# Optimization experiments

Hardware: AMD Instinct MI355X
Metric: run time of the kernel (lower is better)

Reference implementation:

```python
import jax, jax.numpy as jnp
import numpy as np

B, IN_DIM, H1, H2, C = 8192, 1024, 2048, 2048, 1000
E, TOP_K, RH = 8, 2, 512
QB = 127.0
EPS = 1e-5


def _ste_round(x):
    # straight-through estimator round (BitNet-style)
    return x + jax.lax.stop_gradient(jnp.round(x) - x)


def _act_quant(x):
    # per-token absmax 8-bit activation quantization
    s = QB / jnp.clip(jnp.max(jnp.abs(x), axis=-1, keepdims=True), EPS, None)
    return jnp.clip(_ste_round(x * s), -QB, QB) / s


def _weight_quant(w):
    # ternary 1.58b weight quantization, per-tensor mean-abs scale
    s = jnp.clip(jnp.mean(jnp.abs(w)), EPS, None)
    return jnp.clip(_ste_round(w / s), -1.0, 1.0) * s


def _bit_linear(x, w, b):
    return _act_quant(x) @ _weight_quant(w).T + b


def setup_inputs() -> dict:
    key = jax.random.key(0)
    ks = jax.random.split(key, 12)
    def init(k, shape, fan_in):
        return (jax.random.normal(k, shape, dtype=jnp.float32) / np.sqrt(fan_in)).astype(jnp.float32)
    return {
        "x":  jax.random.normal(ks[0], (B, IN_DIM), dtype=jnp.float32),
        "Wr1": init(ks[1], (RH, IN_DIM), IN_DIM),
        "br1": jnp.zeros((RH,), jnp.float32),
        "Wr2": init(ks[2], (E, RH), RH),
        "br2": jnp.zeros((E,), jnp.float32),
        "W1": init(ks[3], (E, H1, IN_DIM), IN_DIM),
        "b1": jnp.zeros((E, H1), jnp.float32),
        "W2": init(ks[4], (E, H2, H1), H1),
        "b2": jnp.zeros((E, H2), jnp.float32),
        "W3": init(ks[5], (E, C, H2), H2),
        "b3": jnp.zeros((E, C), jnp.float32),
    }


def _forward(x, Wr1, br1, Wr2, br2, W1, b1, W2, b2, W3, b3):
    # Router (eval mode: dropout off)
    h = jax.nn.relu(x @ Wr1.T + br1)
    router_probs = jax.nn.softmax(h @ Wr2.T + br2, axis=1)       # [B, E]
    topk_vals, topk_idx = jax.lax.top_k(router_probs, TOP_K)     # [B, K]

    # dense gate matrix: gate[b,e] = sum_k topk_vals[b,k] * (topk_idx[b,k]==e)
    gates = jnp.sum(topk_vals[..., None] * jax.nn.one_hot(topk_idx, E, dtype=x.dtype), axis=1)  # [B, E]

    def expert(w1, c1, w2, c2, w3, c3):
        y = jax.nn.relu(_bit_linear(x, w1, c1))
        y = jax.nn.relu(_bit_linear(y, w2, c2))
        return _bit_linear(y, w3, c3)                             # [B, C]

    out_all = jax.vmap(expert)(W1, b1, W2, b2, W3, b3)            # [E, B, C]
    outputs = jnp.einsum('ebc,be->bc', out_all, gates) / TOP_K    # [B, C]
    load_balancing_loss = jnp.zeros((), x.dtype)                  # eval mode
    return outputs, router_probs, load_balancing_loss


def reference(x, Wr1, br1, Wr2, br2, W1, b1, W2, b2, W3, b3):
    return _forward(x, Wr1, br1, Wr2, br2, W1, b1, W2, b2, W3, b3)
```

## Files before the change

### kernel.cpp

```cpp
#include <hip/hip_runtime.h>
#include <stdint.h>

#define DEV static __device__ __forceinline__

typedef int v4i __attribute__((ext_vector_type(4)));
typedef short v8s __attribute__((ext_vector_type(8)));
typedef float v4f __attribute__((ext_vector_type(4)));

constexpr int B_T   = 8192;
constexpr int IN_D  = 1024;
constexpr int H1D   = 2048;
constexpr int H2D   = 2048;
constexpr int CDIM  = 1000;
constexpr int NEXP  = 8;
constexpr int RHD   = 512;
constexpr float QBF  = 127.0f;
constexpr float EPSF = 1e-5f;
constexpr int NSLOT = 2 * B_T;
constexpr int MAXT  = 136;
constexpr float GAP_DELTA = 2e-3f;

DEV void load_lds16(const void* g, void* l) {
  __builtin_amdgcn_global_load_lds(
      (const __attribute__((address_space(1))) uint32_t*)(uintptr_t)g,
      (__attribute__((address_space(3))) uint32_t*)(uint32_t)(uintptr_t)l,
      16, 0, 0);
}

DEV uint32_t pack4(float a, float b, float c, float d, float s) {
  int q0 = (int)rintf(a * s); q0 = q0 > 127 ? 127 : (q0 < -127 ? -127 : q0);
  int q1 = (int)rintf(b * s); q1 = q1 > 127 ? 127 : (q1 < -127 ? -127 : q1);
  int q2 = (int)rintf(c * s); q2 = q2 > 127 ? 127 : (q2 < -127 ? -127 : q2);
  int q3 = (int)rintf(d * s); q3 = q3 > 127 ? 127 : (q3 < -127 ? -127 : q3);
  return (uint32_t)(uint8_t)q0 | ((uint32_t)(uint8_t)q1 << 8) |
         ((uint32_t)(uint8_t)q2 << 16) | ((uint32_t)(uint8_t)q3 << 24);
}

DEV uint16_t f2bf(float f) {
  uint32_t u = __float_as_uint(f);
  return (uint16_t)((u + 0x7FFFu + ((u >> 16) & 1u)) >> 16);
}
DEV float bf2f(uint16_t h) { return __uint_as_float((uint32_t)h << 16); }

__global__ __launch_bounds__(256) void wabs_reduce(const float* __restrict__ W,
                                                   long perExpert, int tbase,
                                                   double* __restrict__ partial) {
  int e = blockIdx.y;
  const float4* base = (const float4*)(W + (long)e * perExpert);
  long n4 = perExpert >> 2;
  double s = 0.0;
  for (long i = (long)blockIdx.x * 256 + threadIdx.x; i < n4; i += 32L * 256L) {
    float4 v = base[i];
    s += (double)fabsf(v.x) + (double)fabsf(v.y) + (double)fabsf(v.z) + (double)fabsf(v.w);
  }
  __shared__ double red[256];
  red[threadIdx.x] = s;
  __syncthreads();
  for (int st = 128; st > 0; st >>= 1) {
    if ((int)threadIdx.x < st) red[threadIdx.x] += red[threadIdx.x + st];
    __syncthreads();
  }
  if (threadIdx.x == 0) partial[(long)(tbase + e) * 32 + blockIdx.x] = red[0];
}

__global__ void finalize_scales(const double* __restrict__ partial, float* __restrict__ swf) {
  int t = threadIdx.x;
  if (t >= 24) return;
  double s = 0.0;
  for (int i = 0; i < 32; ++i) s += partial[t * 32 + i];
  long cnt = (t < 8) ? (long)H1D * IN_D : (t < 16) ? (long)H2D * H1D : (long)CDIM * H2D;
  float mean = (float)(s / (double)cnt);
  swf[t] = fmaxf(mean, EPSF);
}

__global__ __launch_bounds__(256) void wquant(const float* __restrict__ W,
                                              int8_t* __restrict__ Wq,
                                              const float* __restrict__ swf, int tbase,
                                              long perExpert, long total4) {
  long i = (long)blockIdx.x * 256 + threadIdx.x;
  if (i >= total4) return;
  long e = (i * 4) / perExpert;
  float s = swf[tbase + (int)e];
  float4 v = ((const float4*)W)[i];
  float t0 = fminf(fmaxf(rintf(v.x / s), -1.f), 1.f);
  float t1 = fminf(fmaxf(rintf(v.y / s), -1.f), 1.f);
  float t2 = fminf(fmaxf(rintf(v.z / s), -1.f), 1.f);
  float t3 = fminf(fmaxf(rintf(v.w / s), -1.f), 1.f);
  uint32_t p = (uint32_t)(uint8_t)(int8_t)t0 | ((uint32_t)(uint8_t)(int8_t)t1 << 8) |
               ((uint32_t)(uint8_t)(int8_t)t2 << 16) | ((uint32_t)(uint8_t)(int8_t)t3 << 24);
  ((uint32_t*)Wq)[i] = p;
}

template <int WIDTH>
__global__ __launch_bounds__(256) void actquant(const float* __restrict__ X,
                                                int8_t* __restrict__ Xq,
                                                float* __restrict__ rcp_out) {
  constexpr int PT = WIDTH / 1024;
  const int row = blockIdx.x;
  const int tid = threadIdx.x;
  const float4* src = (const float4*)(X + (size_t)row * WIDTH);
  float4 v[PT];
  float mx = 0.f;
#pragma unroll
  for (int p = 0; p < PT; ++p) {
    v[p] = src[tid * PT + p];
    mx = fmaxf(mx, fmaxf(fmaxf(fabsf(v[p].x), fabsf(v[p].y)),
                         fmaxf(fabsf(v[p].z), fabsf(v[p].w))));
  }
#pragma unroll
  for (int m = 1; m < 64; m <<= 1) mx = fmaxf(mx, __shfl_xor(mx, m));
  __shared__ float wmax[4];
  const int lane = tid & 63, w = tid >> 6;
  if (lane == 0) wmax[w] = mx;
  __syncthreads();
  mx = fmaxf(fmaxf(wmax[0], wmax[1]), fmaxf(wmax[2], wmax[3]));
  const float M = fmaxf(mx, EPSF);
  const float s = QBF / M;
  uint32_t* dst = (uint32_t*)(Xq + (size_t)row * WIDTH);
#pragma unroll
  for (int p = 0; p < PT; ++p)
    dst[tid * PT + p] = pack4(v[p].x, v[p].y, v[p].z, v[p].w, s);
  if (tid == 0) rcp_out[row] = M / QBF;
}

__global__ __launch_bounds__(256) void split_bf16(const float* __restrict__ src,
                                                  uint16_t* __restrict__ hi,
                                                  uint16_t* __restrict__ lo, long n4) {
  long i = (long)blockIdx.x * 256 + threadIdx.x;
  if (i >= n4) return;
  float4 v = ((const float4*)src)[i];
  ushort4 h, l;
  float f[4] = {v.x, v.y, v.z, v.w};
  uint16_t hh[4], ll[4];
#pragma unroll
  for (int j = 0; j < 4; ++j) {
    hh[j] = f2bf(f[j]);
    ll[j] = f2bf(f[j] - bf2f(hh[j]));
  }
  h.x = hh[0]; h.y = hh[1]; h.z = hh[2]; h.w = hh[3];
  l.x = ll[0]; l.y = ll[1]; l.z = ll[2]; l.w = ll[3];
  ((ushort4*)hi)[i] = h;
  ((ushort4*)lo)[i] = l;
}

__global__ __launch_bounds__(256, 1) void router_mfma(
    const uint16_t* __restrict__ xh, const uint16_t* __restrict__ xl,
    const uint16_t* __restrict__ wh, const uint16_t* __restrict__ wl,
    const float* __restrict__ br1, float* __restrict__ h) {
  __shared__ __align__(16) int8_t smem[2][65536];
  const int tid = threadIdx.x;
  const int lane = tid & 63, wid = tid >> 6;
  const int wm = wid >> 1, wn = wid & 1;
  const int row0 = blockIdx.x * 128, col0 = blockIdx.y * 128;

  const uint16_t* mats[4] = {xh, xl, wh, wl};
  const int rb[4] = {row0, row0, col0, col0};
  const uint8_t* src[16];
#pragma unroll
  for (int R = 0; R < 4; ++R)
#pragma unroll
    for (int i = 0; i < 4; ++i) {
      int p = i * 256 + tid;
      int r = p >> 3, c = p & 7;
      int cs = c ^ (r & 7);
      src[R * 4 + i] = (const uint8_t*)mats[R] + ((long)(rb[R] + r) * IN_D + cs * 8) * 2;
    }

  v4f acc[4][4] = {};
  auto stage = [&](int buf, int kt) {
#pragma unroll
    for (int R = 0; R < 4; ++R)
#pragma unroll
      for (int i = 0; i < 4; ++i)
        load_lds16(src[R * 4 + i] + kt * 128,
                   &smem[buf][R * 16384 + i * 4096 + wid * 1024]);
  };

  stage(0, 0);
  asm volatile("s_waitcnt vmcnt(0)" ::: "memory");
  __syncthreads();
  int buf = 0;
  for (int kt = 0; kt < 16; ++kt) {
    if (kt + 1 < 16) stage(buf ^ 1, kt + 1);
#pragma unroll
    for (int ks = 0; ks < 2; ++ks) {
      v8s ah[4], al[4], bh[4], bl[4];
#pragma unroll
      for (int m = 0; m < 4; ++m) {
        int r = wm * 64 + m * 16 + (lane & 15);
        int ch = (ks * 4 + (lane >> 4)) ^ (r & 7);
        ah[m] = *(const v8s*)&smem[buf][r * 128 + ch * 16];
        al[m] = *(const v8s*)&smem[buf][16384 + r * 128 + ch * 16];
      }
#pragma unroll
      for (int n = 0; n < 4; ++n) {
        int r = wn * 64 + n * 16 + (lane & 15);
        int ch = (ks * 4 + (lane >> 4)) ^ (r & 7);
        bh[n] = *(const v8s*)&smem[buf][32768 + r * 128 + ch * 16];
        bl[n] = *(const v8s*)&smem[buf][49152 + r * 128 + ch * 16];
      }
#pragma unroll
      for (int m = 0; m < 4; ++m)
#pragma unroll
        for (int n = 0; n < 4; ++n) {
          acc[m][n] = __builtin_amdgcn_mfma_f32_16x16x32_bf16(ah[m], bh[n], acc[m][n], 0, 0, 0);
          acc[m][n] = __builtin_amdgcn_mfma_f32_16x16x32_bf16(ah[m], bl[n], acc[m][n], 0, 0, 0);
          acc[m][n] = __builtin_amdgcn_mfma_f32_16x16x32_bf16(al[m], bh[n], acc[m][n], 0, 0, 0);
        }
    }
    asm volatile("s_waitcnt vmcnt(0)" ::: "memory");
    __syncthreads();
    buf ^= 1;
  }

  const int rbase = (lane >> 4) * 4;
  const int cfr = lane & 15;
#pragma unroll
  for (int m = 0; m < 4; ++m)
#pragma unroll
    for (int rg = 0; rg < 4; ++rg) {
      int row = row0 + wm * 64 + m * 16 + rbase + rg;
#pragma unroll
      for (int n = 0; n < 4; ++n) {
        int col = col0 + wn * 64 + n * 16 + cfr;
        h[(long)row * RHD + col] = fmaxf(acc[m][n][rg] + br1[col], 0.f);
      }
    }
}

__global__ __launch_bounds__(256) void router_stage2(const float* __restrict__ h,
                                                     const float* __restrict__ Wr2,
                                                     const float* __restrict__ br2,
                                                     float* __restrict__ probs,
                                                     int* __restrict__ idxg,
                                                     float* __restrict__ gvg,
                                                     int* __restrict__ scount,
                                                     int* __restrict__ suspects) {
  __shared__ float w2s[NEXP * RHD];
  const int tid = threadIdx.x;
  for (int i = tid; i < NEXP * RHD; i += 256) w2s[i] = Wr2[i];
  __syncthreads();
  const int lane = tid & 63, w = tid >> 6;
  const int b = blockIdx.x * 4 + w;
  const float* hrow = h + (long)b * RHD;
  float4 v0 = *(const float4*)&hrow[lane * 8];
  float4 v1 = *(const float4*)&hrow[lane * 8 + 4];
  float hr[8] = {v0.x, v0.y, v0.z, v0.w, v1.x, v1.y, v1.z, v1.w};
  float lg[8];
#pragma unroll
  for (int e = 0; e < 8; ++e) {
    float p = 0.f;
#pragma unroll
    for (int j = 0; j < 8; ++j) p = fmaf(hr[j], w2s[e * RHD + lane * 8 + j], p);
#pragma unroll
    for (int m = 1; m < 64; m <<= 1) p += __shfl_xor(p, m);
    lg[e] = p + br2[e];
  }
  if (lane == 0) {
    float mx = lg[0];
#pragma unroll
    for (int e = 1; e < 8; ++e) mx = fmaxf(mx, lg[e]);
    float ex[8], sum = 0.f;
#pragma unroll
    for (int e = 0; e < 8; ++e) { ex[e] = expf(lg[e] - mx); sum += ex[e]; }
#pragma unroll
    for (int e = 0; e < 8; ++e) probs[(long)b * 8 + e] = ex[e] / sum;
    int i0 = 0; float b0 = lg[0];
#pragma unroll
    for (int e = 1; e < 8; ++e) if (lg[e] > b0) { b0 = lg[e]; i0 = e; }
    int i1 = -1; float b1v = -3.4e38f;
#pragma unroll
    for (int e = 0; e < 8; ++e) if (e != i0 && lg[e] > b1v) { b1v = lg[e]; i1 = e; }
    float b2v = -3.4e38f;
#pragma unroll
    for (int e = 0; e < 8; ++e) if (e != i0 && e != i1 && lg[e] > b2v) b2v = lg[e];
    idxg[b * 2 + 0] = i0; idxg[b * 2 + 1] = i1;
    gvg[b * 2 + 0] = ex[i0] / sum; gvg[b * 2 + 1] = ex[i1] / sum;
    if (b1v - b2v < GAP_DELTA) {
      int p = atomicAdd(scount, 1);
      if (p < B_T) suspects[p] = b;
    }
  }
}

__global__ __launch_bounds__(256) void router_fixup(const float* __restrict__ x,
                                                    const float* __restrict__ Wr1,
                                                    const float* __restrict__ br1,
                                                    const float* __restrict__ Wr2,
                                                    const float* __restrict__ br2,
                                                    const int* __restrict__ suspects,
                                                    const int* __restrict__ scount,
                                                    float* __restrict__ probs,
                                                    int* __restrict__ idxg,
                                                    float* __restrict__ gvg) {
  __shared__ float xr[IN_D];
  __shared__ float hr[RHD];
  __shared__ float lgs[NEXP];
  const int n = *scount;
  const int tid = threadIdx.x;
  for (int s = blockIdx.x; s < n && s < B_T; s += 128) {
    const int b = suspects[s];
    __syncthreads();
    for (int i = tid; i < IN_D; i += 256) xr[i] = x[(long)b * IN_D + i];
    __syncthreads();
    {
      const int c0 = tid * 2, c1 = tid * 2 + 1;
      const float* w0 = Wr1 + (long)c0 * IN_D;
      const float* w1 = Wr1 + (long)c1 * IN_D;
      float a0 = 0.f, a1 = 0.f;
      for (int k = 0; k < IN_D; ++k) {
        float xv = xr[k];
        a0 = fmaf(xv, w0[k], a0);
        a1 = fmaf(xv, w1[k], a1);
      }
      hr[c0] = fmaxf(a0 + br1[c0], 0.f);
      hr[c1] = fmaxf(a1 + br1[c1], 0.f);
    }
    __syncthreads();
    if (tid < NEXP) {
      const float* w2 = Wr2 + (long)tid * RHD;
      float a = 0.f;
      for (int k = 0; k < RHD; ++k) a = fmaf(hr[k], w2[k], a);
      lgs[tid] = a + br2[tid];
    }
    __syncthreads();
    if (tid == 0) {
      float lg[8];
#pragma unroll
      for (int e = 0; e < 8; ++e) lg[e] = lgs[e];
      float mx = lg[0];
#pragma unroll
      for (int e = 1; e < 8; ++e) mx = fmaxf(mx, lg[e]);
      float ex[8], sum = 0.f;
#pragma unroll
      for (int e = 0; e < 8; ++e) { ex[e] = expf(lg[e] - mx); sum += ex[e]; }
#pragma unroll
      for (int e = 0; e < 8; ++e) probs[(long)b * 8 + e] = ex[e] / sum;
      int i0 = 0; float b0 = lg[0];
#pragma unroll
      for (int e = 1; e < 8; ++e) if (lg[e] > b0) { b0 = lg[e]; i0 = e; }
      int i1 = -1; float b1v = -3.4e38f;
#pragma unroll
      for (int e = 0; e < 8; ++e) if (e != i0 && lg[e] > b1v) { b1v = lg[e]; i1 = e; }
      idxg[b * 2 + 0] = i0; idxg[b * 2 + 1] = i1;
      gvg[b * 2 + 0] = ex[i0] / sum; gvg[b * 2 + 1] = ex[i1] / sum;
    }
  }
}

__global__ __launch_bounds__(256) void hist_block(const int* __restrict__ idxg,
                                                  int* __restrict__ bc) {
  __shared__ int hloc[NEXP];
  const int t = threadIdx.x;
  if (t < NEXP) hloc[t] = 0;
  __syncthreads();
  int a = blockIdx.x * 256 + t;
  atomicAdd(&hloc[idxg[a]], 1);
  __syncthreads();
  if (t < NEXP) bc[blockIdx.x * NEXP + t] = hloc[t];
}

__global__ void scan_all(const int* __restrict__ bc, int* __restrict__ blockbase,
                         int* __restrict__ ntiles, int* __restrict__ te,
                         int* __restrict__ ts, int* __restrict__ tc,
                         float* __restrict__ loss_out) {
  __shared__ int counts[NEXP], basep[NEXP];
  const int t = threadIdx.x;
  if (t < NEXP) {
    int s = 0;
    for (int b = 0; b < 64; ++b) s += bc[b * NEXP + t];
    counts[t] = s;
  }
  __syncthreads();
  if (t == 0) {
    int acc = 0, nb = 0;
    for (int e = 0; e < NEXP; ++e) {
      basep[e] = acc;
      int c = counts[e];
      int nt = (c + 127) >> 7;
      for (int i = 0; i < nt; ++i) {
        te[nb] = e; ts[nb] = acc + i * 128; tc[nb] = min(128, c - i * 128); ++nb;
      }
      acc += c;
    }
    *ntiles = nb;
    *loss_out = 0.f;
  }
  __syncthreads();
  if (t < NEXP) {
    int run = basep[t];
    for (int b = 0; b < 64; ++b) { blockbase[b * NEXP + t] = run; run += bc[b * NEXP + t]; }
  }
}

__global__ __launch_bounds__(256) void place2(const int* __restrict__ idxg,
                                              const int* __restrict__ blockbase,
                                              int* __restrict__ token_list,
                                              int* __restrict__ slotmap) {
  __shared__ int cur[NEXP];
  const int t = threadIdx.x;
  if (t < NEXP) cur[t] = blockbase[blockIdx.x * NEXP + t];
  __syncthreads();
  int a = blockIdx.x * 256 + t;
  int e = idxg[a];
  int pos = atomicAdd(&cur[e], 1);
  token_list[pos] = a >> 1;
  slotmap[a] = pos;
}

template <int KDIM, bool INDIRECT, bool RELU, bool FINAL>
__global__ __launch_bounds__(256, 2) void gemm_i8(
    const int8_t* __restrict__ Aq, const int8_t* __restrict__ Wq,
    const float* __restrict__ swf_layer, const float* __restrict__ rcp_act,
    const float* __restrict__ bias, const int* __restrict__ te,
    const int* __restrict__ ts, const int* __restrict__ tc,
    const int* __restrict__ ntiles_p, const int* __restrict__ token_list,
    float* __restrict__ Yout, int Nvalid) {
  if ((int)blockIdx.x >= *ntiles_p) return;
  __shared__ __align__(16) int8_t smem[2][16384];
  const int t = blockIdx.x;
  const int e = te[t], row0 = ts[t], rcount = tc[t];
  const int col0 = blockIdx.y * 128;
  const int tid = threadIdx.x;
  const int lane = tid & 63, wid = tid >> 6;
  const int wm = wid >> 1, wn = wid & 1;

  const int8_t* srcA[2];
  const int8_t* srcB[2];
#pragma unroll
  for (int i = 0; i < 2; ++i) {
    int p = tid + i * 256;
    int r = p >> 2, c = p & 3;
    int cs = c ^ ((r >> 1) & 3);
    int ar = row0 + min(r, rcount - 1);
    long arow = INDIRECT ? (long)token_list[ar] : (long)ar;
    srcA[i] = Aq + arow * KDIM + cs * 16;
    int br = min(col0 + r, Nvalid - 1);
    srcB[i] = Wq + ((long)e * Nvalid + br) * (long)KDIM + cs * 16;
  }

  v4i acc[4][4] = {};
  auto stage = [&](int buf, int kt) {
#pragma unroll
    for (int i = 0; i < 2; ++i) {
      int off = (i * 256 + wid * 64) * 16;
      load_lds16(srcA[i] + kt * 64, &smem[buf][off]);
      load_lds16(srcB[i] + kt * 64, &smem[buf][8192 + off]);
    }
  };

  constexpr int KT = KDIM / 64;
  stage(0, 0);
  asm volatile("s_waitcnt vmcnt(0)" ::: "memory");
  __syncthreads();
  int buf = 0;
  for (int kt = 0; kt < KT; ++kt) {
    if (kt + 1 < KT) stage(buf ^ 1, kt + 1);
    const v4i* As = (const v4i*)&smem[buf][0];
    const v4i* Bs = (const v4i*)&smem[buf][8192];
    v4i av[4], bv[4];
#pragma unroll
    for (int m = 0; m < 4; ++m) {
      int r = wm * 64 + m * 16 + (lane & 15);
      av[m] = As[r * 4 + ((lane >> 4) ^ ((r >> 1) & 3))];
    }
#pragma unroll
    for (int n = 0; n < 4; ++n) {
      int r = wn * 64 + n * 16 + (lane & 15);
      bv[n] = Bs[r * 4 + ((lane >> 4) ^ ((r >> 1) & 3))];
    }
#pragma unroll
    for (int m = 0; m < 4; ++m)
#pragma unroll
      for (int n = 0; n < 4; ++n)
        acc[m][n] = __builtin_amdgcn_mfma_i32_16x16x64_i8(av[m], bv[n], acc[m][n], 0, 0, 0);
    asm volatile("s_waitcnt vmcnt(0)" ::: "memory");
    __syncthreads();
    buf ^= 1;
  }

  const float sw = swf_layer[e];
  const int rbase = (lane >> 4) * 4;
  const int cfr = lane & 15;
  const float* bias_e = bias + (long)e * Nvalid;
#pragma unroll
  for (int m = 0; m < 4; ++m) {
#pragma unroll
    for (int rg = 0; rg < 4; ++rg) {
      int trow = wm * 64 + m * 16 + rbase + rg;
      if (trow >= rcount) continue;
      int slot = row0 + trow;
      float rcp = rcp_act[INDIRECT ? token_list[slot] : slot];
      float dq = sw * rcp;
      if (!FINAL) {
        float* yrow = Yout + (long)slot * 2048;
#pragma unroll
        for (int n = 0; n < 4; ++n) {
          int o = col0 + wn * 64 + n * 16 + cfr;
          float v = (float)acc[m][n][rg] * dq + bias_e[o];
          if (RELU) v = fmaxf(v, 0.f);
          yrow[o] = v;
        }
      } else {
        float* zrow = Yout + (long)slot * 1024;
#pragma unroll
        for (int n = 0; n < 4; ++n) {
          int o = col0 + wn * 64 + n * 16 + cfr;
          float bb = bias_e[min(o, Nvalid - 1)];
          zrow[o] = (float)acc[m][n][rg] * dq + bb;
        }
      }
    }
  }
}

__global__ __launch_bounds__(256) void combine(const float* __restrict__ z,
                                               const int* __restrict__ slotmap,
                                               const float* __restrict__ gvg,
                                               float* __restrict__ out) {
  const int b = blockIdx.x;
  const int c = threadIdx.x;
  if (c >= 250) return;
  const int s0 = slotmap[b * 2], s1 = slotmap[b * 2 + 1];
  const float g0 = gvg[b * 2] * 0.5f, g1 = gvg[b * 2 + 1] * 0.5f;
  float4 a = *(const float4*)(z + (long)s0 * 1024 + c * 4);
  float4 q = *(const float4*)(z + (long)s1 * 1024 + c * 4);
  float4 o = {g0 * a.x + g1 * q.x, g0 * a.y + g1 * q.y,
              g0 * a.z + g1 * q.z, g0 * a.w + g1 * q.w};
  *(float4*)(out + (long)b * CDIM + c * 4) = o;
}

extern "C" void kernel_launch(void* const* d_in, const int* in_sizes, int n_in,
                              void* d_out, int out_size, void* d_ws, size_t ws_size,
                              hipStream_t stream) {
  const float* x   = (const float*)d_in[0];
  const float* Wr1 = (const float*)d_in[1];
  const float* br1 = (const float*)d_in[2];
  const float* Wr2 = (const float*)d_in[3];
  const float* br2 = (const float*)d_in[4];
  const float* W1  = (const float*)d_in[5];
  const float* b1  = (const float*)d_in[6];
  const float* W2  = (const float*)d_in[7];
  const float* b2  = (const float*)d_in[8];
  const float* W3  = (const float*)d_in[9];
  const float* b3  = (const float*)d_in[10];
  float* out = (float*)d_out;
  char* ws = (char*)d_ws;

  size_t off = 0;
  auto alloc = [&](size_t sz) { size_t r = off; off = (off + sz + 255) & ~(size_t)255; return r; };
  size_t O_META  = alloc(8192);
  size_t O_SUSP  = alloc(B_T * sizeof(int));
  size_t O_PART  = alloc(24 * 32 * sizeof(double));
  size_t O_SWF   = alloc(24 * sizeof(float));
  size_t O_RCPX  = alloc(B_T * sizeof(float));
  size_t O_IDX   = alloc(B_T * 2 * sizeof(int));
  size_t O_GVG   = alloc(B_T * 2 * sizeof(float));
  size_t O_TLIST = alloc(NSLOT * sizeof(int));
  size_t O_SLOT  = alloc(B_T * 2 * sizeof(int));
  size_t O_S1    = alloc(NSLOT * sizeof(float));
  size_t O_S2    = alloc(NSLOT * sizeof(float));
  size_t O_XQ    = alloc((size_t)B_T * IN_D);
  size_t O_WQ1   = alloc((size_t)NEXP * H1D * IN_D);
  size_t O_WQ2   = alloc((size_t)NEXP * H2D * H1D);
  size_t O_WQ3   = alloc((size_t)NEXP * CDIM * H2D);
  size_t O_YQ    = alloc((size_t)NSLOT * 2048);
  size_t O_YBIG  = alloc((size_t)NSLOT * 2048 * sizeof(float));
  (void)ws_size; (void)in_sizes; (void)n_in;

  int*    te     = (int*)(ws + O_META);
  int*    tsv    = te + 144;
  int*    tcv    = tsv + 144;
  int*    ntiles = tcv + 144;
  int*    bc     = ntiles + 4;
  int*    bbase  = bc + 512;
  int*    scount = bbase + 512;
  int*    susp   = (int*)(ws + O_SUSP);
  double* part   = (double*)(ws + O_PART);
  float*  swf    = (float*)(ws + O_SWF);
  float*  rcpx   = (float*)(ws + O_RCPX);
  int*    idxg   = (int*)(ws + O_IDX);
  float*  gvg    = (float*)(ws + O_GVG);
  int*    tlist  = (int*)(ws + O_TLIST);
  int*    slotmap= (int*)(ws + O_SLOT);
  float*  s1     = (float*)(ws + O_S1);
  float*  s2     = (float*)(ws + O_S2);
  int8_t* Xq     = (int8_t*)(ws + O_XQ);
  int8_t* wq1    = (int8_t*)(ws + O_WQ1);
  int8_t* wq2    = (int8_t*)(ws + O_WQ2);
  int8_t* wq3    = (int8_t*)(ws + O_WQ3);
  int8_t* Yq     = (int8_t*)(ws + O_YQ);
  float*  Ybig   = (float*)(ws + O_YBIG);
  float*  h      = Ybig;
  float*  zbuf   = Ybig;

  char* ybytes = (char*)Ybig;
  uint16_t* xh = (uint16_t*)(ybytes + (20l << 20));
  uint16_t* xl = (uint16_t*)(ybytes + (40l << 20));
  uint16_t* wh = (uint16_t*)(ybytes + (60l << 20));
  uint16_t* wl = (uint16_t*)(ybytes + (62l << 20));

  hipMemsetAsync(ws + O_META, 0, 8192, stream);

  wabs_reduce<<<dim3(32, 8), 256, 0, stream>>>(W1, (long)H1D * IN_D, 0, part);
  wabs_reduce<<<dim3(32, 8), 256, 0, stream>>>(W2, (long)H2D * H1D, 8, part);
  wabs_reduce<<<dim3(32, 8), 256, 0, stream>>>(W3, (long)CDIM * H2D, 16, part);
  finalize_scales<<<1, 64, 0, stream>>>(part, swf);
  wquant<<<16384, 256, 0, stream>>>(W1, wq1, swf, 0, (long)H1D * IN_D, 4194304L);
  wquant<<<32768, 256, 0, stream>>>(W2, wq2, swf, 8, (long)H2D * H1D, 8388608L);
  wquant<<<16000, 256, 0, stream>>>(W3, wq3, swf, 16, (long)CDIM * H2D, 4096000L);

  actquant<IN_D><<<B_T, 256, 0, stream>>>(x, Xq, rcpx);

  split_bf16<<<8192, 256, 0, stream>>>(x, xh, xl, (long)B_T * IN_D / 4);
  split_bf16<<<512, 256, 0, stream>>>(Wr1, wh, wl, (long)RHD * IN_D / 4);
  router_mfma<<<dim3(B_T / 128, RHD / 128), 256, 0, stream>>>(xh, xl, wh, wl, br1, h);
  router_stage2<<<B_T / 4, 256, 0, stream>>>(h, Wr2, br2, out + (size_t)B_T * CDIM,
                                             idxg, gvg, scount, susp);
  router_fixup<<<128, 256, 0, stream>>>(x, Wr1, br1, Wr2, br2, susp, scount,
                                        out + (size_t)B_T * CDIM, idxg, gvg);
  hist_block<<<64, 256, 0, stream>>>(idxg, bc);
  scan_all<<<1, 64, 0, stream>>>(bc, bbase, ntiles, te, tsv, tcv,
                                 out + (size_t)B_T * CDIM + (size_t)B_T * NEXP);
  place2<<<64, 256, 0, stream>>>(idxg, bbase, tlist, slotmap);

  gemm_i8<IN_D, true, true, false><<<dim3(MAXT, H1D / 128), 256, 0, stream>>>(
      Xq, wq1, swf + 0, rcpx, b1, te, tsv, tcv, ntiles, tlist, Ybig, H1D);
  actquant<2048><<<NSLOT, 256, 0, stream>>>(Ybig, Yq, s1);
  gemm_i8<2048, false, true, false><<<dim3(MAXT, H2D / 128), 256, 0, stream>>>(
      Yq, wq2, swf + 8, s1, b2, te, tsv, tcv, ntiles, tlist, Ybig, H2D);
  actquant<2048><<<NSLOT, 256, 0, stream>>>(Ybig, Yq, s2);
  gemm_i8<2048, false, false, true><<<dim3(MAXT, 1024 / 128), 256, 0, stream>>>(
      Yq, wq3, swf + 16, s2, b3, te, tsv, tcv, ntiles, tlist, zbuf, CDIM);

  combine<<<B_T, 256, 0, stream>>>(zbuf, slotmap, gvg, out);
}
```

Measured before the change: 688.5 us.

## Enlarge int8 GEMM tiles to 256x256x128 with 512 threads and dynamic LDS

The grouped int8 expert GEMMs move from 128x128 tiles with K-step 64 and 256 threads to 256x256 tiles with K-step 128 and 512 threads (8 waves, each computing 128x64). Double-buffered LDS grows to 128 KB of dynamic shared memory, and routing now groups tokens into 256-row tiles per expert. The loop uses a partial vmcnt wait plus sched barriers so the next stage's loads overlap compute. The aim is more operand reuse per byte loaded. The cost is fewer blocks (lower occupancy, one block per CU), more padding waste in per-expert tiles, and a dependence on the 160 KB LDS available on MI355X.

```diff
diff --git a/kernel.cpp b/kernel.cpp
--- a/kernel.cpp
+++ b/kernel.cpp
@@ -17,7 +17,7 @@
 constexpr float QBF  = 127.0f;
 constexpr float EPSF = 1e-5f;
 constexpr int NSLOT = 2 * B_T;
-constexpr int MAXT  = 136;
+constexpr int MAXT  = 72;
 constexpr float GAP_DELTA = 2e-3f;
 
 DEV void load_lds16(const void* g, void* l) {
@@ -377,9 +377,9 @@
     for (int e = 0; e < NEXP; ++e) {
       basep[e] = acc;
       int c = counts[e];
-      int nt = (c + 127) >> 7;
+      int nt = (c + 255) >> 8;
       for (int i = 0; i < nt; ++i) {
-        te[nb] = e; ts[nb] = acc + i * 128; tc[nb] = min(128, c - i * 128); ++nb;
+        te[nb] = e; ts[nb] = acc + i * 256; tc[nb] = min(256, c - i * 256); ++nb;
       }
       acc += c;
     }
@@ -409,7 +409,7 @@
 }
 
 template <int KDIM, bool INDIRECT, bool RELU, bool FINAL>
-__global__ __launch_bounds__(256, 2) void gemm_i8(
+__global__ __launch_bounds__(512, 1) void gemm_i8(
     const int8_t* __restrict__ Aq, const int8_t* __restrict__ Wq,
     const float* __restrict__ swf_layer, const float* __restrict__ rcp_act,
     const float* __restrict__ bias, const int* __restrict__ te,
@@ -417,21 +417,21 @@
     const int* __restrict__ ntiles_p, const int* __restrict__ token_list,
     float* __restrict__ Yout, int Nvalid) {
   if ((int)blockIdx.x >= *ntiles_p) return;
-  __shared__ __align__(16) int8_t smem[2][16384];
+  extern __shared__ __align__(16) int8_t smem_dyn[];
   const int t = blockIdx.x;
   const int e = te[t], row0 = ts[t], rcount = tc[t];
-  const int col0 = blockIdx.y * 128;
+  const int col0 = blockIdx.y * 256;
   const int tid = threadIdx.x;
   const int lane = tid & 63, wid = tid >> 6;
-  const int wm = wid >> 1, wn = wid & 1;
-
-  const int8_t* srcA[2];
-  const int8_t* srcB[2];
-#pragma unroll
-  for (int i = 0; i < 2; ++i) {
-    int p = tid + i * 256;
-    int r = p >> 2, c = p & 3;
-    int cs = c ^ ((r >> 1) & 3);
+  const int wm = wid >> 2, wn = wid & 3;
+
+  const int8_t* srcA[4];
+  const int8_t* srcB[4];
+#pragma unroll
+  for (int i = 0; i < 4; ++i) {
+    int p = i * 512 + tid;
+    int r = p >> 3, c = p & 7;
+    int cs = c ^ ((r >> 1) & 7);
     int ar = row0 + min(r, rcount - 1);
     long arow = INDIRECT ? (long)token_list[ar] : (long)ar;
     srcA[i] = Aq + arow * KDIM + cs * 16;
@@ -439,43 +439,53 @@
     srcB[i] = Wq + ((long)e * Nvalid + br) * (long)KDIM + cs * 16;
   }
 
-  v4i acc[4][4] = {};
   auto stage = [&](int buf, int kt) {
 #pragma unroll
-    for (int i = 0; i < 2; ++i) {
-      int off = (i * 256 + wid * 64) * 16;
-      load_lds16(srcA[i] + kt * 64, &smem[buf][off]);
-      load_lds16(srcB[i] + kt * 64, &smem[buf][8192 + off]);
+    for (int i = 0; i < 4; ++i) {
+      int off = buf * 65536 + (i * 512 + (wid << 6)) * 16;
+      load_lds16(srcA[i] + kt * 128, &smem_dyn[off]);
+      load_lds16(srcB[i] + kt * 128, &smem_dyn[32768 + off]);
     }
   };
 
-  constexpr int KT = KDIM / 64;
+  v4i acc[8][4] = {};
+  constexpr int KT = KDIM / 128;
   stage(0, 0);
   asm volatile("s_waitcnt vmcnt(0)" ::: "memory");
-  __syncthreads();
+  __builtin_amdgcn_s_barrier();
   int buf = 0;
   for (int kt = 0; kt < KT; ++kt) {
-    if (kt + 1 < KT) stage(buf ^ 1, kt + 1);
-    const v4i* As = (const v4i*)&smem[buf][0];
-    const v4i* Bs = (const v4i*)&smem[buf][8192];
-    v4i av[4], bv[4];
-#pragma unroll
-    for (int m = 0; m < 4; ++m) {
-      int r = wm * 64 + m * 16 + (lane & 15);
-      av[m] = As[r * 4 + ((lane >> 4) ^ ((r >> 1) & 3))];
-    }
-#pragma unroll
-    for (int n = 0; n < 4; ++n) {
-      int r = wn * 64 + n * 16 + (lane & 15);
-      bv[n] = Bs[r * 4 + ((lane >> 4) ^ ((r >> 1) & 3))];
-    }
-#pragma unroll
-    for (int m = 0; m < 4; ++m)
-#pragma unroll
-      for (int n = 0; n < 4; ++n)
-        acc[m][n] = __builtin_amdgcn_mfma_i32_16x16x64_i8(av[m], bv[n], acc[m][n], 0, 0, 0);
-    asm volatile("s_waitcnt vmcnt(0)" ::: "memory");
-    __syncthreads();
+    if (kt + 1 < KT) {
+      stage(buf ^ 1, kt + 1);
+      asm volatile("s_waitcnt vmcnt(8)" ::: "memory");
+    } else {
+      asm volatile("s_waitcnt vmcnt(0)" ::: "memory");
+    }
+    __builtin_amdgcn_s_barrier();
+    __builtin_amdgcn_sched_barrier(0);
+    const int8_t* As = &smem_dyn[buf * 65536];
+    const int8_t* Bs = &smem_dyn[buf * 65536 + 32768];
+#pragma unroll
+    for (int ks = 0; ks < 2; ++ks) {
+      v4i bv[4];
+#pragma unroll
+      for (int n = 0; n < 4; ++n) {
+        int r = wn * 64 + n * 16 + (lane & 15);
+        int cs = (ks * 4 + (lane >> 4)) ^ ((r >> 1) & 7);
+        bv[n] = *(const v4i*)&Bs[r * 128 + cs * 16];
+      }
+#pragma unroll
+      for (int m = 0; m < 8; ++m) {
+        int r = wm * 128 + m * 16 + (lane & 15);
+        int cs = (ks * 4 + (lane >> 4)) ^ ((r >> 1) & 7);
+        v4i av = *(const v4i*)&As[r * 128 + cs * 16];
+#pragma unroll
+        for (int n = 0; n < 4; ++n)
+          acc[m][n] = __builtin_amdgcn_mfma_i32_16x16x64_i8(av, bv[n], acc[m][n], 0, 0, 0);
+      }
+    }
+    __builtin_amdgcn_sched_barrier(0);
+    __builtin_amdgcn_s_barrier();
     buf ^= 1;
   }
 
@@ -484,10 +494,10 @@
   const int cfr = lane & 15;
   const float* bias_e = bias + (long)e * Nvalid;
 #pragma unroll
-  for (int m = 0; m < 4; ++m) {
+  for (int m = 0; m < 8; ++m) {
 #pragma unroll
     for (int rg = 0; rg < 4; ++rg) {
-      int trow = wm * 64 + m * 16 + rbase + rg;
+      int trow = wm * 128 + m * 16 + rbase + rg;
       if (trow >= rcount) continue;
       int slot = row0 + trow;
       float rcp = rcp_act[INDIRECT ? token_list[slot] : slot];
@@ -624,13 +634,13 @@
                                  out + (size_t)B_T * CDIM + (size_t)B_T * NEXP);
   place2<<<64, 256, 0, stream>>>(idxg, bbase, tlist, slotmap);
 
-  gemm_i8<IN_D, true, true, false><<<dim3(MAXT, H1D / 128), 256, 0, stream>>>(
+  gemm_i8<IN_D, true, true, false><<<dim3(MAXT, H1D / 256), 512, 131072, stream>>>(
       Xq, wq1, swf + 0, rcpx, b1, te, tsv, tcv, ntiles, tlist, Ybig, H1D);
   actquant<2048><<<NSLOT, 256, 0, stream>>>(Ybig, Yq, s1);
-  gemm_i8<2048, false, true, false><<<dim3(MAXT, H2D / 128), 256, 0, stream>>>(
+  gemm_i8<2048, false, true, false><<<dim3(MAXT, H2D / 256), 512, 131072, stream>>>(
       Yq, wq2, swf + 8, s1, b2, te, tsv, tcv, ntiles, tlist, Ybig, H2D);
   actquant<2048><<<NSLOT, 256, 0, stream>>>(Ybig, Yq, s2);
-  gemm_i8<2048, false, false, true><<<dim3(MAXT, 1024 / 128), 256, 0, stream>>>(
+  gemm_i8<2048, false, false, true><<<dim3(MAXT, 1024 / 256), 512, 131072, stream>>>(
       Yq, wq3, swf + 16, s2, b3, te, tsv, tcv, ntiles, tlist, zbuf, CDIM);
 
   combine<<<B_T, 256, 0, stream>>>(zbuf, slotmap, gvg, out);
```

Result: no change. 690.6 us (+0.3%).
